# Kernel tuning notes

Measured on AMD Instinct MI355X. Metric: run time of the kernel, lower is better.

## Reference

```python
import jax, jax.numpy as jnp
import numpy as np

N_NODES = 100000
N_EDGES = 3200000
IN_C = 128
OUT_C = 40
NEG_SLOPE = 0.2


def _p(key, shape, scale=0.1):
    return jax.random.normal(key, shape, dtype=jnp.float32) * scale


def setup_inputs() -> dict:
    key = jax.random.key(0)
    ks = jax.random.split(key, 16)
    x = jax.random.normal(ks[0], (N_NODES, IN_C), dtype=jnp.float32)
    edge_index = jax.random.randint(ks[1], (2, N_EDGES), 0, N_NODES, dtype=jnp.int32)
    # layer 1: in=128 -> heads=4, out=4 (concat -> 16)
    W1 = _p(ks[2], (IN_C, 4 * 4))
    a_src1 = _p(ks[3], (4, 4))
    a_dst1 = _p(ks[4], (4, 4))
    b1 = jnp.zeros((16,), jnp.float32)
    # layer 2: 16 -> heads=8, out=8 (concat -> 64)
    W2 = _p(ks[5], (16, 8 * 8))
    a_src2 = _p(ks[6], (8, 8))
    a_dst2 = _p(ks[7], (8, 8))
    b2 = jnp.zeros((64,), jnp.float32)
    # layer 3: 64 -> heads=1, out=OUT_C, concat=False
    W3 = _p(ks[8], (64, OUT_C))
    a_src3 = _p(ks[9], (1, OUT_C))
    a_dst3 = _p(ks[10], (1, OUT_C))
    b3 = jnp.zeros((OUT_C,), jnp.float32)
    return {"x": x, "edge_index": edge_index,
            "W1": W1, "a_src1": a_src1, "a_dst1": a_dst1, "b1": b1,
            "W2": W2, "a_src2": a_src2, "a_dst2": a_dst2, "b2": b2,
            "W3": W3, "a_src3": a_src3, "a_dst3": a_dst3, "b3": b3}


def gat_conv(x, src, dst, W, a_src, a_dst, b, heads, out_c, concat):
    # x: [N, F_in]; src/dst: [E] (self loops already included)
    N = x.shape[0]
    h = (x @ W).reshape(N, heads, out_c)                 # [N, H, C]
    e_src = jnp.sum(h * a_src, axis=-1)                  # [N, H]
    e_dst = jnp.sum(h * a_dst, axis=-1)                  # [N, H]
    e = jax.nn.leaky_relu(e_src[src] + e_dst[dst], NEG_SLOPE)  # [E, H]
    # segment softmax over edges grouped by destination node
    m = jax.ops.segment_max(e, dst, num_segments=N)      # [N, H]
    ex = jnp.exp(e - m[dst])
    s = jax.ops.segment_sum(ex, dst, num_segments=N)
    alpha = ex / (s[dst] + 1e-16)                        # [E, H]
    out = jax.ops.segment_sum(h[src] * alpha[:, :, None], dst, num_segments=N)  # [N, H, C]
    out = out.reshape(N, heads * out_c) if concat else out.mean(axis=1)
    return out + b


def reference(x, edge_index, W1, a_src1, a_dst1, b1, W2, a_src2, a_dst2, b2, W3, a_src3, a_dst3, b3):
    N = x.shape[0]
    loops = jnp.arange(N, dtype=edge_index.dtype)
    src = jnp.concatenate([edge_index[0], loops])
    dst = jnp.concatenate([edge_index[1], loops])
    h = jax.nn.elu(gat_conv(x, src, dst, W1, a_src1, a_dst1, b1, 4, 4, True))
    h = jax.nn.elu(gat_conv(h, src, dst, W2, a_src2, a_dst2, b2, 8, 8, True))
    out = gat_conv(h, src, dst, W3, a_src3, a_dst3, b3, 1, OUT_C, False)
    return out
```

## Files before the change

kernel.cpp:

```cpp
#include <hip/hip_runtime.h>

#define NN 100000
#define NE 3200000
#define ET (NE + NN)
#define NEG_SLOPE 0.2f
#define BSH 7
#define WIN (1 << BSH)
#define NBUC ((NN + WIN - 1) >> BSH)
#define NBLK 256
#define EPB ((ET + NBLK - 1) / NBLK)

__device__ __host__ __forceinline__ int swz(int b) {
    return (b & 7) * (NBLK / 8) + (b >> 3);
}

__device__ __forceinline__ float lrelu(float v) { return v > 0.f ? v : NEG_SLOPE * v; }

__device__ __forceinline__ unsigned short f2bf(float x) {
    unsigned u = __float_as_uint(x);
    return (unsigned short)((u + 0x7fffu + ((u >> 16) & 1u)) >> 16);
}
__device__ __forceinline__ float bflo(unsigned u) { return __uint_as_float(u << 16); }
__device__ __forceinline__ float bfhi(unsigned u) { return __uint_as_float(u & 0xffff0000u); }


__global__ __launch_bounds__(1024) void cnt_kernel(const int* __restrict__ dst,
                                                   int* __restrict__ cnt) {
    __shared__ int h[NBUC];
    for (int i = threadIdx.x; i < NBUC; i += 1024) h[i] = 0;
    __syncthreads();
    int lo = blockIdx.x * EPB;
    int hi = lo + EPB; if (hi > ET) hi = ET;
    for (int k = lo + threadIdx.x; k < hi; k += 1024) {
        int d = (k < NE) ? dst[k] : k - NE;
        atomicAdd(&h[d >> BSH], 1);
    }
    __syncthreads();
    int col = swz(blockIdx.x);
    for (int i = threadIdx.x; i < NBUC; i += 1024)
        cnt[i * NBLK + col] = h[i];
}

__global__ __launch_bounds__(256) void rowsum_kernel(const int* __restrict__ cnt,
                                                     int* __restrict__ tot) {
    int wave = threadIdx.x >> 6, lane = threadIdx.x & 63;
    int b = blockIdx.x * 4 + wave;
    if (b >= NBUC) return;
    int4 v = ((const int4*)(cnt + b * NBLK))[lane];
    int s = v.x + v.y + v.z + v.w;
#pragma unroll
    for (int off = 32; off; off >>= 1) s += __shfl_xor(s, off);
    if (lane == 0) tot[b] = s;
}

__global__ __launch_bounds__(1024) void scan_kernel(const int* __restrict__ tot,
                                                    int* __restrict__ bstart) {
    __shared__ int t[1024];
    int b = threadIdx.x;
    int s = (b < NBUC) ? tot[b] : 0;
    t[b] = s;
    __syncthreads();
    for (int off = 1; off < 1024; off <<= 1) {
        int v = (b >= off) ? t[b - off] : 0;
        __syncthreads();
        t[b] += v;
        __syncthreads();
    }
    if (b < NBUC) bstart[b] = t[b] - s;
    if (b == 0) bstart[NBUC] = ET;
}

__global__ __launch_bounds__(256) void base_kernel(int* __restrict__ cnt,
                                                   const int* __restrict__ bstart) {
    int wave = threadIdx.x >> 6, lane = threadIdx.x & 63;
    int b = blockIdx.x * 4 + wave;
    if (b >= NBUC) return;
    int run = bstart[b];
    for (int c0 = 0; c0 < NBLK; c0 += 64) {
        int v = cnt[b * NBLK + c0 + lane];
        int x = v;
#pragma unroll
        for (int off = 1; off < 64; off <<= 1) {
            int y = __shfl_up(x, off);
            if (lane >= off) x += y;
        }
        cnt[b * NBLK + c0 + lane] = run + x - v;
        run += __shfl(x, 63);
    }
}

__global__ __launch_bounds__(1024) void scatter_kernel(const int* __restrict__ src,
                                                       const int* __restrict__ dst,
                                                       const int* __restrict__ base,
                                                       unsigned* __restrict__ tmpp) {
    __shared__ int loff[NBUC];
    int col = swz(blockIdx.x);
    for (int i = threadIdx.x; i < NBUC; i += 1024) loff[i] = base[i * NBLK + col];
    __syncthreads();
    int lo = blockIdx.x * EPB;
    int hi = lo + EPB; if (hi > ET) hi = ET;
    for (int k = lo + threadIdx.x; k < hi; k += 1024) {
        int s, d;
        if (k < NE) { s = src[k]; d = dst[k]; }
        else { s = d = k - NE; }
        int p = atomicAdd(&loff[d >> BSH], 1);
        tmpp[p] = (unsigned)s | ((unsigned)(d & (WIN - 1)) << 17);
    }
}

__global__ __launch_bounds__(512) void sort_kernel(const int* __restrict__ bstart,
                                                   const unsigned* __restrict__ tmpp,
                                                   int* __restrict__ rowptr,
                                                   int* __restrict__ ssrc) {
    __shared__ int hist[WIN];
    __shared__ int scan[WIN];
    __shared__ int cur[WIN];
    int buc = blockIdx.x;
    int nlo = buc << BSH;
    int nwin = NN - nlo; if (nwin > WIN) nwin = WIN;
    int lo = bstart[buc], hi = bstart[buc + 1];
    int tid = threadIdx.x;
    if (tid < WIN) hist[tid] = 0;
    __syncthreads();
    for (int k = lo + tid; k < hi; k += 512)
        atomicAdd(&hist[tmpp[k] >> 17], 1);
    __syncthreads();
    if (tid < WIN) scan[tid] = hist[tid];
    __syncthreads();
    for (int off = 1; off < WIN; off <<= 1) {
        int v = (tid >= off && tid < WIN) ? scan[tid - off] : 0;
        __syncthreads();
        if (tid < WIN) scan[tid] += v;
        __syncthreads();
    }
    if (tid < WIN) {
        int ex = scan[tid] - hist[tid];
        cur[tid] = ex;
        if (tid < nwin) rowptr[nlo + tid] = lo + ex;
    }
    if (buc == 0 && tid == 0) rowptr[NN] = ET;
    __syncthreads();
    for (int k = lo + tid; k < hi; k += 512) {
        unsigned e = tmpp[k];
        int p = atomicAdd(&cur[e >> 17], 1);
        ssrc[lo + p] = (int)(e & 0x1FFFFu);
    }
}


template <int FIN, int FOUT, int C>
__global__ __launch_bounds__(256) void gemm_attn_kernel(
    const float* __restrict__ x, const float* __restrict__ W,
    const float* __restrict__ a_src, const float* __restrict__ a_dst,
    unsigned short* __restrict__ h, float* __restrict__ esrc,
    float* __restrict__ edst, int N) {
    constexpr int HH = FOUT / C;
    constexpr int F4 = FOUT / 4;
    constexpr int TPH = C / 4;
    __shared__ __align__(16) float Ws[FIN * FOUT];
    for (int i = threadIdx.x; i < FIN * FOUT; i += blockDim.x) Ws[i] = W[i];
    __syncthreads();
    int idx = blockIdx.x * blockDim.x + threadIdx.x;
    if (idx >= N * F4) return;
    int n = idx / F4, f4 = idx - n * F4;
    int fb = 4 * f4;
    const float4* xr = (const float4*)(x + (long)n * FIN);
    float a0 = 0.f, a1 = 0.f, a2 = 0.f, a3 = 0.f;
#pragma unroll
    for (int k4 = 0; k4 < FIN / 4; ++k4) {
        float4 xv = xr[k4];
        const float* wr = &Ws[(4 * k4) * FOUT + fb];
        float4 w0 = *(const float4*)(wr);
        float4 w1 = *(const float4*)(wr + FOUT);
        float4 w2 = *(const float4*)(wr + 2 * FOUT);
        float4 w3 = *(const float4*)(wr + 3 * FOUT);
        a0 = fmaf(xv.x, w0.x, a0); a1 = fmaf(xv.x, w0.y, a1);
        a2 = fmaf(xv.x, w0.z, a2); a3 = fmaf(xv.x, w0.w, a3);
        a0 = fmaf(xv.y, w1.x, a0); a1 = fmaf(xv.y, w1.y, a1);
        a2 = fmaf(xv.y, w1.z, a2); a3 = fmaf(xv.y, w1.w, a3);
        a0 = fmaf(xv.z, w2.x, a0); a1 = fmaf(xv.z, w2.y, a1);
        a2 = fmaf(xv.z, w2.z, a2); a3 = fmaf(xv.z, w2.w, a3);
        a0 = fmaf(xv.w, w3.x, a0); a1 = fmaf(xv.w, w3.y, a1);
        a2 = fmaf(xv.w, w3.z, a2); a3 = fmaf(xv.w, w3.w, a3);
    }
    unsigned short b0 = f2bf(a0), b1 = f2bf(a1), b2 = f2bf(a2), b3 = f2bf(a3);
    *(ushort4*)(h + (long)n * FOUT + fb) = make_ushort4(b0, b1, b2, b3);
    float q0 = bflo((unsigned)b0), q1 = bflo((unsigned)b1);
    float q2 = bflo((unsigned)b2), q3 = bflo((unsigned)b3);
    float vs = q0 * a_src[fb] + q1 * a_src[fb + 1] + q2 * a_src[fb + 2] + q3 * a_src[fb + 3];
    float vd = q0 * a_dst[fb] + q1 * a_dst[fb + 1] + q2 * a_dst[fb + 2] + q3 * a_dst[fb + 3];
#pragma unroll
    for (int o = 1; o < TPH; o <<= 1) {
        vs += __shfl_xor(vs, o);
        vd += __shfl_xor(vd, o);
    }
    if ((f4 % TPH) == 0) {
        int hh = f4 / TPH;
        esrc[n * HH + hh] = vs;
        edst[n * HH + hh] = vd;
    }
}

template <int FIN, int FOUT, int SO>
__global__ __launch_bounds__(256) void gemm_kernel(const float* __restrict__ x,
                                                   const float* __restrict__ W,
                                                   unsigned short* __restrict__ h, int N) {
    constexpr int F4 = FOUT / 4;
    __shared__ __align__(16) float Ws[FIN * FOUT];
    for (int i = threadIdx.x; i < FIN * FOUT; i += blockDim.x) Ws[i] = W[i];
    __syncthreads();
    int idx = blockIdx.x * blockDim.x + threadIdx.x;
    if (idx >= N * F4) return;
    int n = idx / F4, f4 = idx - n * F4;
    int fb = 4 * f4;
    const float4* xr = (const float4*)(x + (long)n * FIN);
    float a0 = 0.f, a1 = 0.f, a2 = 0.f, a3 = 0.f;
#pragma unroll
    for (int k4 = 0; k4 < FIN / 4; ++k4) {
        float4 xv = xr[k4];
        const float* wr = &Ws[(4 * k4) * FOUT + fb];
        float4 w0 = *(const float4*)(wr);
        float4 w1 = *(const float4*)(wr + FOUT);
        float4 w2 = *(const float4*)(wr + 2 * FOUT);
        float4 w3 = *(const float4*)(wr + 3 * FOUT);
        a0 = fmaf(xv.x, w0.x, a0); a1 = fmaf(xv.x, w0.y, a1);
        a2 = fmaf(xv.x, w0.z, a2); a3 = fmaf(xv.x, w0.w, a3);
        a0 = fmaf(xv.y, w1.x, a0); a1 = fmaf(xv.y, w1.y, a1);
        a2 = fmaf(xv.y, w1.z, a2); a3 = fmaf(xv.y, w1.w, a3);
        a0 = fmaf(xv.z, w2.x, a0); a1 = fmaf(xv.z, w2.y, a1);
        a2 = fmaf(xv.z, w2.z, a2); a3 = fmaf(xv.z, w2.w, a3);
        a0 = fmaf(xv.w, w3.x, a0); a1 = fmaf(xv.w, w3.y, a1);
        a2 = fmaf(xv.w, w3.z, a2); a3 = fmaf(xv.w, w3.w, a3);
    }
    *(ushort4*)(h + (long)n * SO + fb) = make_ushort4(f2bf(a0), f2bf(a1), f2bf(a2), f2bf(a3));
}

template <int C, int SO>
__global__ void attn_kernel(const unsigned short* __restrict__ h,
                            const float* __restrict__ a_src,
                            const float* __restrict__ a_dst, float* __restrict__ esrc,
                            float* __restrict__ edst, int N) {
    int idx = blockIdx.x * blockDim.x + threadIdx.x;
    if (idx >= N) return;
    const uint4* hp = (const uint4*)(h + (long)idx * SO);
    float s = 0.f, d = 0.f;
#pragma unroll
    for (int c8 = 0; c8 < C / 8; ++c8) {
        uint4 v = hp[c8];
        int c = 8 * c8;
        s += bflo(v.x) * a_src[c] + bfhi(v.x) * a_src[c + 1];
        d += bflo(v.x) * a_dst[c] + bfhi(v.x) * a_dst[c + 1];
        s += bflo(v.y) * a_src[c + 2] + bfhi(v.y) * a_src[c + 3];
        d += bflo(v.y) * a_dst[c + 2] + bfhi(v.y) * a_dst[c + 3];
        s += bflo(v.z) * a_src[c + 4] + bfhi(v.z) * a_src[c + 5];
        d += bflo(v.z) * a_dst[c + 4] + bfhi(v.z) * a_dst[c + 5];
        s += bflo(v.w) * a_src[c + 6] + bfhi(v.w) * a_src[c + 7];
        d += bflo(v.w) * a_dst[c + 6] + bfhi(v.w) * a_dst[c + 7];
    }
    esrc[idx] = s;
    edst[idx] = d;
}

template <int H, int C, int L, int G, int NPW, int FPL, int RSL, int U, bool ELU>
__global__ __launch_bounds__(256) void agg_kernel(
    const int* __restrict__ rowptr, const int* __restrict__ ssrc,
    const float* __restrict__ esrc, const float* __restrict__ edst,
    const unsigned short* __restrict__ hbuf, const float* __restrict__ b,
    float* __restrict__ out, int N) {
    constexpr int F = H * C;
    constexpr int AQ = (F + FPL - 1) / FPL;
    constexpr int S = L * G;
    static_assert(S * NPW == 64, "wave layout");
    static_assert(AQ <= L, "lanes cover features");
    int lane = threadIdx.x & 63;
    int wave = threadIdx.x >> 6;
    int sub = lane / S;
    int ls = lane - sub * S;
    int g = ls / L, q = ls - g * L;
    int n = (blockIdx.x * 4 + wave) * NPW + sub;
    if (n >= N) return;
    const bool act = (q < AQ);
    int h = act ? (FPL * q) / C : 0;
    int qa = act ? q : 0;
    float edn = edst[n * H + h];
    int beg = rowptr[n], end = rowptr[n + 1];
    int kend = end - 1;
    float sum = 0.f;
    float acc[FPL];
#pragma unroll
    for (int i = 0; i < FPL; ++i) acc[i] = 0.f;

    int k = beg + g;
    int ss[U];
#pragma unroll
    for (int u = 0; u < U; ++u) {
        int kk = k + u * G;
        ss[u] = ssrc[kk < kend ? kk : kend];
    }
    while (k < end) {
        uint4 hv4[U];
        uint2 hv2[U];
        float es[U];
#pragma unroll
        for (int u = 0; u < U; ++u) {
            if constexpr (FPL == 8) hv4[u] = ((const uint4*)hbuf)[ss[u] * RSL + qa];
            else hv2[u] = ((const uint2*)hbuf)[ss[u] * RSL + qa];
            es[u] = esrc[ss[u] * H + h];
        }
        int kn = k + U * G;
        int sn[U];
#pragma unroll
        for (int u = 0; u < U; ++u) {
            int kk = kn + u * G;
            sn[u] = ssrc[kk < kend ? kk : kend];
        }
        __builtin_amdgcn_sched_barrier(0);
#pragma unroll
        for (int u = 0; u < U; ++u) {
            float ex = (act && (k + u * G < end)) ? __expf(lrelu(es[u] + edn)) : 0.f;
            if constexpr (FPL == 8) {
                uint4 v = hv4[u];
                acc[0] = fmaf(ex, bflo(v.x), acc[0]); acc[1] = fmaf(ex, bfhi(v.x), acc[1]);
                acc[2] = fmaf(ex, bflo(v.y), acc[2]); acc[3] = fmaf(ex, bfhi(v.y), acc[3]);
                acc[4] = fmaf(ex, bflo(v.z), acc[4]); acc[5] = fmaf(ex, bfhi(v.z), acc[5]);
                acc[6] = fmaf(ex, bflo(v.w), acc[6]); acc[7] = fmaf(ex, bfhi(v.w), acc[7]);
            } else {
                uint2 v = hv2[u];
                acc[0] = fmaf(ex, bflo(v.x), acc[0]); acc[1] = fmaf(ex, bfhi(v.x), acc[1]);
                acc[2] = fmaf(ex, bflo(v.y), acc[2]); acc[3] = fmaf(ex, bfhi(v.y), acc[3]);
            }
            sum += ex;
        }
#pragma unroll
        for (int u = 0; u < U; ++u) ss[u] = sn[u];
        k = kn;
    }
#pragma unroll
    for (int step = L; step < S; step <<= 1) {
        sum += __shfl_xor(sum, step);
#pragma unroll
        for (int i = 0; i < FPL; ++i) acc[i] += __shfl_xor(acc[i], step);
    }
    if (g == 0 && act) {
        float inv = 1.f / (sum + 1e-16f);
        float v[FPL];
#pragma unroll
        for (int i = 0; i < FPL; ++i) {
            v[i] = acc[i] * inv + b[FPL * q + i];
            if (ELU) v[i] = v[i] > 0.f ? v[i] : __expf(v[i]) - 1.f;
        }
        float* op = out + n * F + FPL * q;
#pragma unroll
        for (int i = 0; i < FPL; i += 4)
            *(float4*)(op + i) = make_float4(v[i], v[i + 1], v[i + 2], v[i + 3]);
    }
}

static inline int cdiv(long a, int b) { return (int)((a + b - 1) / b); }

extern "C" void kernel_launch(void* const* d_in, const int* in_sizes, int n_in,
                              void* d_out, int out_size, void* d_ws, size_t ws_size,
                              hipStream_t stream) {
    const float* x1 = (const float*)d_in[0];
    const int* ei = (const int*)d_in[1];
    const int* src = ei;
    const int* dst = ei + NE;
    const float* W1 = (const float*)d_in[2];
    const float* as1 = (const float*)d_in[3];
    const float* ad1 = (const float*)d_in[4];
    const float* b1 = (const float*)d_in[5];
    const float* W2 = (const float*)d_in[6];
    const float* as2 = (const float*)d_in[7];
    const float* ad2 = (const float*)d_in[8];
    const float* b2 = (const float*)d_in[9];
    const float* W3 = (const float*)d_in[10];
    const float* as3 = (const float*)d_in[11];
    const float* ad3 = (const float*)d_in[12];
    const float* b3 = (const float*)d_in[13];
    float* out = (float*)d_out;

    char* wsb = (char*)d_ws;
    unsigned short* hbuf = (unsigned short*)wsb;  wsb += (long)NN * 64 * 2;
    float* x2 = (float*)wsb;         wsb += (long)NN * 16 * 4;
    float* x3 = (float*)wsb;         wsb += (long)NN * 64 * 4;
    float* esrc = (float*)wsb;       wsb += (long)NN * 8 * 4;
    float* edst = (float*)wsb;       wsb += (long)NN * 8 * 4;
    unsigned* tmpp = (unsigned*)wsb; wsb += (long)ET * 4;
    int* ssrc = (int*)wsb;           wsb += (long)ET * 4;
    int* rowptr = (int*)wsb;         wsb += (long)(NN + 1) * 4;
    int* cnt = (int*)wsb;            wsb += (long)NBUC * NBLK * 4;
    int* bstart = (int*)wsb;         wsb += (long)(NBUC + 1) * 4;
    int* tot = (int*)wsb;            wsb += (long)NBUC * 4;

    const int B = 256;

    cnt_kernel<<<NBLK, 1024, 0, stream>>>(dst, cnt);
    rowsum_kernel<<<cdiv(NBUC, 4), B, 0, stream>>>(cnt, tot);
    scan_kernel<<<1, 1024, 0, stream>>>(tot, bstart);
    base_kernel<<<cdiv(NBUC, 4), B, 0, stream>>>(cnt, bstart);
    scatter_kernel<<<NBLK, 1024, 0, stream>>>(src, dst, cnt, tmpp);
    sort_kernel<<<NBUC, 512, 0, stream>>>(bstart, tmpp, rowptr, ssrc);

    gemm_attn_kernel<128, 16, 4><<<cdiv((long)NN * 4, B), B, 0, stream>>>(
        x1, W1, as1, ad1, hbuf, esrc, edst, NN);
    agg_kernel<4, 4, 4, 8, 2, 4, 4, 5, true><<<cdiv(NN, 8), B, 0, stream>>>(
        rowptr, ssrc, esrc, edst, hbuf, b1, x2, NN);

    gemm_attn_kernel<16, 64, 8><<<cdiv((long)NN * 16, B), B, 0, stream>>>(
        x2, W2, as2, ad2, hbuf, esrc, edst, NN);
    agg_kernel<8, 8, 8, 8, 1, 8, 8, 5, true><<<cdiv(NN, 4), B, 0, stream>>>(
        rowptr, ssrc, esrc, edst, hbuf, b2, x3, NN);

    gemm_kernel<64, 40, 40><<<cdiv((long)NN * 10, B), B, 0, stream>>>(x3, W3, hbuf, NN);
    attn_kernel<40, 40><<<cdiv(NN, B), B, 0, stream>>>(hbuf, as3, ad3, esrc, edst, NN);
    agg_kernel<1, 40, 8, 8, 1, 8, 5, 5, false><<<cdiv(NN, 4), B, 0, stream>>>(
        rowptr, ssrc, esrc, edst, hbuf, b3, out, NN);
}
```

Baseline: 424.9 us.

## Fuse destination counting with layer-1 GEMM into one heterogeneous launch

Merges the edge-bucket counting kernel and the first-layer GEMM plus attention-score kernel into a single launch. The first 256 blocks do the histogram and the rest do the GEMM, so the two independent stages can overlap and one launch goes away. The counting blocks drop from 1024 to 256 threads. Separately, the sort kernel moves to 1024 threads and the last template parameter of all agg kernels changes from 5 to 6. Mixing two workloads in one grid may leave the histogram blocks running longer and unbalance the grid.

```diff
diff --git a/kernel.cpp b/kernel.cpp
--- a/kernel.cpp
+++ b/kernel.cpp
@@ -24,143 +24,15 @@
 __device__ __forceinline__ float bfhi(unsigned u) { return __uint_as_float(u & 0xffff0000u); }
 
 
-__global__ __launch_bounds__(1024) void cnt_kernel(const int* __restrict__ dst,
-                                                   int* __restrict__ cnt) {
-    __shared__ int h[NBUC];
-    for (int i = threadIdx.x; i < NBUC; i += 1024) h[i] = 0;
-    __syncthreads();
-    int lo = blockIdx.x * EPB;
-    int hi = lo + EPB; if (hi > ET) hi = ET;
-    for (int k = lo + threadIdx.x; k < hi; k += 1024) {
-        int d = (k < NE) ? dst[k] : k - NE;
-        atomicAdd(&h[d >> BSH], 1);
-    }
-    __syncthreads();
-    int col = swz(blockIdx.x);
-    for (int i = threadIdx.x; i < NBUC; i += 1024)
-        cnt[i * NBLK + col] = h[i];
-}
-
-__global__ __launch_bounds__(256) void rowsum_kernel(const int* __restrict__ cnt,
-                                                     int* __restrict__ tot) {
-    int wave = threadIdx.x >> 6, lane = threadIdx.x & 63;
-    int b = blockIdx.x * 4 + wave;
-    if (b >= NBUC) return;
-    int4 v = ((const int4*)(cnt + b * NBLK))[lane];
-    int s = v.x + v.y + v.z + v.w;
-#pragma unroll
-    for (int off = 32; off; off >>= 1) s += __shfl_xor(s, off);
-    if (lane == 0) tot[b] = s;
-}
-
-__global__ __launch_bounds__(1024) void scan_kernel(const int* __restrict__ tot,
-                                                    int* __restrict__ bstart) {
-    __shared__ int t[1024];
-    int b = threadIdx.x;
-    int s = (b < NBUC) ? tot[b] : 0;
-    t[b] = s;
-    __syncthreads();
-    for (int off = 1; off < 1024; off <<= 1) {
-        int v = (b >= off) ? t[b - off] : 0;
-        __syncthreads();
-        t[b] += v;
-        __syncthreads();
-    }
-    if (b < NBUC) bstart[b] = t[b] - s;
-    if (b == 0) bstart[NBUC] = ET;
-}
-
-__global__ __launch_bounds__(256) void base_kernel(int* __restrict__ cnt,
-                                                   const int* __restrict__ bstart) {
-    int wave = threadIdx.x >> 6, lane = threadIdx.x & 63;
-    int b = blockIdx.x * 4 + wave;
-    if (b >= NBUC) return;
-    int run = bstart[b];
-    for (int c0 = 0; c0 < NBLK; c0 += 64) {
-        int v = cnt[b * NBLK + c0 + lane];
-        int x = v;
-#pragma unroll
-        for (int off = 1; off < 64; off <<= 1) {
-            int y = __shfl_up(x, off);
-            if (lane >= off) x += y;
-        }
-        cnt[b * NBLK + c0 + lane] = run + x - v;
-        run += __shfl(x, 63);
-    }
-}
-
-__global__ __launch_bounds__(1024) void scatter_kernel(const int* __restrict__ src,
-                                                       const int* __restrict__ dst,
-                                                       const int* __restrict__ base,
-                                                       unsigned* __restrict__ tmpp) {
-    __shared__ int loff[NBUC];
-    int col = swz(blockIdx.x);
-    for (int i = threadIdx.x; i < NBUC; i += 1024) loff[i] = base[i * NBLK + col];
-    __syncthreads();
-    int lo = blockIdx.x * EPB;
-    int hi = lo + EPB; if (hi > ET) hi = ET;
-    for (int k = lo + threadIdx.x; k < hi; k += 1024) {
-        int s, d;
-        if (k < NE) { s = src[k]; d = dst[k]; }
-        else { s = d = k - NE; }
-        int p = atomicAdd(&loff[d >> BSH], 1);
-        tmpp[p] = (unsigned)s | ((unsigned)(d & (WIN - 1)) << 17);
-    }
-}
-
-__global__ __launch_bounds__(512) void sort_kernel(const int* __restrict__ bstart,
-                                                   const unsigned* __restrict__ tmpp,
-                                                   int* __restrict__ rowptr,
-                                                   int* __restrict__ ssrc) {
-    __shared__ int hist[WIN];
-    __shared__ int scan[WIN];
-    __shared__ int cur[WIN];
-    int buc = blockIdx.x;
-    int nlo = buc << BSH;
-    int nwin = NN - nlo; if (nwin > WIN) nwin = WIN;
-    int lo = bstart[buc], hi = bstart[buc + 1];
-    int tid = threadIdx.x;
-    if (tid < WIN) hist[tid] = 0;
-    __syncthreads();
-    for (int k = lo + tid; k < hi; k += 512)
-        atomicAdd(&hist[tmpp[k] >> 17], 1);
-    __syncthreads();
-    if (tid < WIN) scan[tid] = hist[tid];
-    __syncthreads();
-    for (int off = 1; off < WIN; off <<= 1) {
-        int v = (tid >= off && tid < WIN) ? scan[tid - off] : 0;
-        __syncthreads();
-        if (tid < WIN) scan[tid] += v;
-        __syncthreads();
-    }
-    if (tid < WIN) {
-        int ex = scan[tid] - hist[tid];
-        cur[tid] = ex;
-        if (tid < nwin) rowptr[nlo + tid] = lo + ex;
-    }
-    if (buc == 0 && tid == 0) rowptr[NN] = ET;
-    __syncthreads();
-    for (int k = lo + tid; k < hi; k += 512) {
-        unsigned e = tmpp[k];
-        int p = atomicAdd(&cur[e >> 17], 1);
-        ssrc[lo + p] = (int)(e & 0x1FFFFu);
-    }
-}
-
-
 template <int FIN, int FOUT, int C>
-__global__ __launch_bounds__(256) void gemm_attn_kernel(
-    const float* __restrict__ x, const float* __restrict__ W,
+__device__ __forceinline__ void gemm_attn_body(
+    int idx, const float* __restrict__ x, const float* Ws,
     const float* __restrict__ a_src, const float* __restrict__ a_dst,
     unsigned short* __restrict__ h, float* __restrict__ esrc,
     float* __restrict__ edst, int N) {
     constexpr int HH = FOUT / C;
     constexpr int F4 = FOUT / 4;
     constexpr int TPH = C / 4;
-    __shared__ __align__(16) float Ws[FIN * FOUT];
-    for (int i = threadIdx.x; i < FIN * FOUT; i += blockDim.x) Ws[i] = W[i];
-    __syncthreads();
-    int idx = blockIdx.x * blockDim.x + threadIdx.x;
     if (idx >= N * F4) return;
     int n = idx / F4, f4 = idx - n * F4;
     int fb = 4 * f4;
@@ -199,6 +71,158 @@
         esrc[n * HH + hh] = vs;
         edst[n * HH + hh] = vd;
     }
+}
+
+
+__global__ __launch_bounds__(256) void cntgemm_kernel(
+    const int* __restrict__ dst, int* __restrict__ cnt,
+    const float* __restrict__ x, const float* __restrict__ W,
+    const float* __restrict__ a_src, const float* __restrict__ a_dst,
+    unsigned short* __restrict__ h, float* __restrict__ esrc,
+    float* __restrict__ edst, int N) {
+    __shared__ __align__(16) char smem[128 * 16 * 4];
+    if (blockIdx.x < NBLK) {
+        int* hh = (int*)smem;
+        for (int i = threadIdx.x; i < NBUC; i += 256) hh[i] = 0;
+        __syncthreads();
+        int lo = blockIdx.x * EPB;
+        int hi = lo + EPB; if (hi > ET) hi = ET;
+        for (int k = lo + threadIdx.x; k < hi; k += 256) {
+            int d = (k < NE) ? dst[k] : k - NE;
+            atomicAdd(&hh[d >> BSH], 1);
+        }
+        __syncthreads();
+        int col = swz(blockIdx.x);
+        for (int i = threadIdx.x; i < NBUC; i += 256)
+            cnt[i * NBLK + col] = hh[i];
+    } else {
+        float* Ws = (float*)smem;
+        for (int i = threadIdx.x; i < 128 * 16; i += 256) Ws[i] = W[i];
+        __syncthreads();
+        int idx = (blockIdx.x - NBLK) * 256 + threadIdx.x;
+        gemm_attn_body<128, 16, 4>(idx, x, Ws, a_src, a_dst, h, esrc, edst, N);
+    }
+}
+
+
+__global__ __launch_bounds__(256) void rowsum_kernel(const int* __restrict__ cnt,
+                                                     int* __restrict__ tot) {
+    int wave = threadIdx.x >> 6, lane = threadIdx.x & 63;
+    int b = blockIdx.x * 4 + wave;
+    if (b >= NBUC) return;
+    int4 v = ((const int4*)(cnt + b * NBLK))[lane];
+    int s = v.x + v.y + v.z + v.w;
+#pragma unroll
+    for (int off = 32; off; off >>= 1) s += __shfl_xor(s, off);
+    if (lane == 0) tot[b] = s;
+}
+
+__global__ __launch_bounds__(1024) void scan_kernel(const int* __restrict__ tot,
+                                                    int* __restrict__ bstart) {
+    __shared__ int t[1024];
+    int b = threadIdx.x;
+    int s = (b < NBUC) ? tot[b] : 0;
+    t[b] = s;
+    __syncthreads();
+    for (int off = 1; off < 1024; off <<= 1) {
+        int v = (b >= off) ? t[b - off] : 0;
+        __syncthreads();
+        t[b] += v;
+        __syncthreads();
+    }
+    if (b < NBUC) bstart[b] = t[b] - s;
+    if (b == 0) bstart[NBUC] = ET;
+}
+
+__global__ __launch_bounds__(256) void base_kernel(int* __restrict__ cnt,
+                                                   const int* __restrict__ bstart) {
+    int wave = threadIdx.x >> 6, lane = threadIdx.x & 63;
+    int b = blockIdx.x * 4 + wave;
+    if (b >= NBUC) return;
+    int run = bstart[b];
+    for (int c0 = 0; c0 < NBLK; c0 += 64) {
+        int v = cnt[b * NBLK + c0 + lane];
+        int x = v;
+#pragma unroll
+        for (int off = 1; off < 64; off <<= 1) {
+            int y = __shfl_up(x, off);
+            if (lane >= off) x += y;
+        }
+        cnt[b * NBLK + c0 + lane] = run + x - v;
+        run += __shfl(x, 63);
+    }
+}
+
+__global__ __launch_bounds__(1024) void scatter_kernel(const int* __restrict__ src,
+                                                       const int* __restrict__ dst,
+                                                       const int* __restrict__ base,
+                                                       unsigned* __restrict__ tmpp) {
+    __shared__ int loff[NBUC];
+    int col = swz(blockIdx.x);
+    for (int i = threadIdx.x; i < NBUC; i += 1024) loff[i] = base[i * NBLK + col];
+    __syncthreads();
+    int lo = blockIdx.x * EPB;
+    int hi = lo + EPB; if (hi > ET) hi = ET;
+    for (int k = lo + threadIdx.x; k < hi; k += 1024) {
+        int s, d;
+        if (k < NE) { s = src[k]; d = dst[k]; }
+        else { s = d = k - NE; }
+        int p = atomicAdd(&loff[d >> BSH], 1);
+        tmpp[p] = (unsigned)s | ((unsigned)(d & (WIN - 1)) << 17);
+    }
+}
+
+__global__ __launch_bounds__(1024) void sort_kernel(const int* __restrict__ bstart,
+                                                    const unsigned* __restrict__ tmpp,
+                                                    int* __restrict__ rowptr,
+                                                    int* __restrict__ ssrc) {
+    __shared__ int hist[WIN];
+    __shared__ int scan[WIN];
+    __shared__ int cur[WIN];
+    int buc = blockIdx.x;
+    int nlo = buc << BSH;
+    int nwin = NN - nlo; if (nwin > WIN) nwin = WIN;
+    int lo = bstart[buc], hi = bstart[buc + 1];
+    int tid = threadIdx.x;
+    if (tid < WIN) hist[tid] = 0;
+    __syncthreads();
+    for (int k = lo + tid; k < hi; k += 1024)
+        atomicAdd(&hist[tmpp[k] >> 17], 1);
+    __syncthreads();
+    if (tid < WIN) scan[tid] = hist[tid];
+    __syncthreads();
+    for (int off = 1; off < WIN; off <<= 1) {
+        int v = (tid >= off && tid < WIN) ? scan[tid - off] : 0;
+        __syncthreads();
+        if (tid < WIN) scan[tid] += v;
+        __syncthreads();
+    }
+    if (tid < WIN) {
+        int ex = scan[tid] - hist[tid];
+        cur[tid] = ex;
+        if (tid < nwin) rowptr[nlo + tid] = lo + ex;
+    }
+    if (buc == 0 && tid == 0) rowptr[NN] = ET;
+    __syncthreads();
+    for (int k = lo + tid; k < hi; k += 1024) {
+        unsigned e = tmpp[k];
+        int p = atomicAdd(&cur[e >> 17], 1);
+        ssrc[lo + p] = (int)(e & 0x1FFFFu);
+    }
+}
+
+
+template <int FIN, int FOUT, int C>
+__global__ __launch_bounds__(256) void gemm_attn_kernel(
+    const float* __restrict__ x, const float* __restrict__ W,
+    const float* __restrict__ a_src, const float* __restrict__ a_dst,
+    unsigned short* __restrict__ h, float* __restrict__ esrc,
+    float* __restrict__ edst, int N) {
+    __shared__ __align__(16) float Ws[FIN * FOUT];
+    for (int i = threadIdx.x; i < FIN * FOUT; i += blockDim.x) Ws[i] = W[i];
+    __syncthreads();
+    int idx = blockIdx.x * blockDim.x + threadIdx.x;
+    gemm_attn_body<FIN, FOUT, C>(idx, x, Ws, a_src, a_dst, h, esrc, edst, N);
 }
 
 template <int FIN, int FOUT, int SO>
@@ -394,25 +418,24 @@
 
     const int B = 256;
 
-    cnt_kernel<<<NBLK, 1024, 0, stream>>>(dst, cnt);
+    cntgemm_kernel<<<NBLK + cdiv((long)NN * 4, B), B, 0, stream>>>(
+        dst, cnt, x1, W1, as1, ad1, hbuf, esrc, edst, NN);
     rowsum_kernel<<<cdiv(NBUC, 4), B, 0, stream>>>(cnt, tot);
     scan_kernel<<<1, 1024, 0, stream>>>(tot, bstart);
     base_kernel<<<cdiv(NBUC, 4), B, 0, stream>>>(cnt, bstart);
     scatter_kernel<<<NBLK, 1024, 0, stream>>>(src, dst, cnt, tmpp);
-    sort_kernel<<<NBUC, 512, 0, stream>>>(bstart, tmpp, rowptr, ssrc);
-
-    gemm_attn_kernel<128, 16, 4><<<cdiv((long)NN * 4, B), B, 0, stream>>>(
-        x1, W1, as1, ad1, hbuf, esrc, edst, NN);
-    agg_kernel<4, 4, 4, 8, 2, 4, 4, 5, true><<<cdiv(NN, 8), B, 0, stream>>>(
+    sort_kernel<<<NBUC, 1024, 0, stream>>>(bstart, tmpp, rowptr, ssrc);
+
+    agg_kernel<4, 4, 4, 8, 2, 4, 4, 6, true><<<cdiv(NN, 8), B, 0, stream>>>(
         rowptr, ssrc, esrc, edst, hbuf, b1, x2, NN);
 
     gemm_attn_kernel<16, 64, 8><<<cdiv((long)NN * 16, B), B, 0, stream>>>(
         x2, W2, as2, ad2, hbuf, esrc, edst, NN);
-    agg_kernel<8, 8, 8, 8, 1, 8, 8, 5, true><<<cdiv(NN, 4), B, 0, stream>>>(
+    agg_kernel<8, 8, 8, 8, 1, 8, 8, 6, true><<<cdiv(NN, 4), B, 0, stream>>>(
         rowptr, ssrc, esrc, edst, hbuf, b2, x3, NN);
 
     gemm_kernel<64, 40, 40><<<cdiv((long)NN * 10, B), B, 0, stream>>>(x3, W3, hbuf, NN);
     attn_kernel<40, 40><<<cdiv(NN, B), B, 0, stream>>>(hbuf, as3, ad3, esrc, edst, NN);
-    agg_kernel<1, 40, 8, 8, 1, 8, 5, 5, false><<<cdiv(NN, 4), B, 0, stream>>>(
+    agg_kernel<1, 40, 8, 8, 1, 8, 5, 6, false><<<cdiv(NN, 4), B, 0, stream>>>(
         rowptr, ssrc, esrc, edst, hbuf, b3, out, NN);
 }
```

Result: no change. 430.3 us (+1.3%).
